# Kernel tuning notes

Hardware: AMD Instinct MI355X
Metric: run time of the kernel (lower is better)

## Reference

```python
import jax, jax.numpy as jnp
import numpy as np

NUM_HEADS = 12
HEAD_DIM = 32  # all_head_size(384) / num_heads(12)


def setup_inputs() -> dict:
    key = jax.random.key(0)
    ks = jax.random.split(key, 8)
    B, Sq, Sk, Din, AH = 1, 4096, 4096, 768, 384
    scale = 1.0 / np.sqrt(Din)
    return {
        "hidden_states": jax.random.normal(ks[0], (B, Sq, Din), jnp.float32),
        "encoder_hidden_states": jax.random.normal(ks[1], (B, Sk, Din), jnp.float32),
        "encoder_attention_mask": jnp.zeros((B, 1, 1, Sk), jnp.float32),
        "Wq": jax.random.normal(ks[2], (Din, AH), jnp.float32) * scale,
        "bq": jnp.zeros((AH,), jnp.float32),
        "Wk": jax.random.normal(ks[3], (Din, AH), jnp.float32) * scale,
        "bk": jnp.zeros((AH,), jnp.float32),
        "Wv": jax.random.normal(ks[4], (Din, AH), jnp.float32) * scale,
        "bv": jnp.zeros((AH,), jnp.float32),
    }


def _split_heads(x):
    # [B, S, H*D] -> [B, H, S, D]
    B, S, _ = x.shape
    return x.reshape(B, S, NUM_HEADS, HEAD_DIM).transpose(0, 2, 1, 3)


def reference(hidden_states, encoder_hidden_states, encoder_attention_mask,
              Wq, bq, Wk, bk, Wv, bv):
    q = _split_heads(hidden_states @ Wq + bq)            # [B,H,Sq,D]
    k = _split_heads(encoder_hidden_states @ Wk + bk)    # [B,H,Sk,D]
    v = _split_heads(encoder_hidden_states @ Wv + bv)    # [B,H,Sk,D]

    scores = jnp.einsum('bhqd,bhkd->bhqk', q, k) / np.sqrt(HEAD_DIM)
    scores = scores + encoder_attention_mask              # additive mask, broadcast
    probs = jax.nn.softmax(scores, axis=-1)               # dropout is identity (eval)

    ctx = jnp.einsum('bhqk,bhkd->bhqd', probs, v)         # [B,H,Sq,D]
    B, H, Sq, D = ctx.shape
    return ctx.transpose(0, 2, 1, 3).reshape(B, Sq, H * D)  # [B,Sq,all_head_size]
```

## Files before the change

kernel.cpp:

```cpp
#include <hip/hip_runtime.h>
#include <hip/hip_bf16.h>

#define SQ 4096
#define SKK 4096
#define DIN 768
#define AHS 384
#define NHEAD 12
#define HD 32

typedef __attribute__((ext_vector_type(8))) short bf16x8;
typedef __attribute__((ext_vector_type(4))) float f32x4;
typedef __attribute__((ext_vector_type(4))) unsigned int u32x4;

#define LOG2E 1.4426950408889634f
#define QSCALE 0.25503486168652855f

__device__ __forceinline__ unsigned short bf16_rn(float x){
  unsigned int u = __float_as_uint(x);
  unsigned int r = u + 0x7fffu + ((u>>16)&1u);
  return (unsigned short)(r>>16);
}
__device__ __forceinline__ float bf16_f(unsigned short h){
  return __uint_as_float(((unsigned int)h)<<16);
}
__device__ __forceinline__ float fexp2(float x){
#if __has_builtin(__builtin_amdgcn_exp2f)
  return __builtin_amdgcn_exp2f(x);
#else
  float r; asm("v_exp_f32 %0, %1" : "=v"(r) : "v"(x)); return r;
#endif
}

__global__ void prep_wt_kernel(const float* __restrict__ Wq, const float* __restrict__ Wk,
                               const float* __restrict__ Wv, const float* __restrict__ mask,
                               unsigned short* __restrict__ Wthi, unsigned short* __restrict__ Wtlo,
                               unsigned short* __restrict__ EMB){
  int idx = blockIdx.x*256 + threadIdx.x;
  if (idx < SKK) EMB[idx] = bf16_rn(__expf(mask[idx]));
  const int per = DIN*AHS;
  if (idx >= 3*per) return;
  int mat = idx/per, rem = idx - mat*per;
  int k = rem/AHS, n = rem - k*AHS;
  const float* W = (mat==0)?Wq:((mat==1)?Wk:Wv);
  float v = W[k*AHS+n];
  unsigned short hh = bf16_rn(v);
  unsigned short ll = bf16_rn(v - bf16_f(hh));
  Wthi[mat*per + n*DIN + k] = hh;
  Wtlo[mat*per + n*DIN + k] = ll;
}

__global__ __launch_bounds__(512,4) void proj2_kernel(
    const float* __restrict__ Xh, const float* __restrict__ Xe,
    const unsigned short* __restrict__ Wthi, const unsigned short* __restrict__ Wtlo,
    const float* __restrict__ bq, const float* __restrict__ bk, const float* __restrict__ bv,
    const unsigned short* __restrict__ EMB,
    unsigned short* __restrict__ Qhi, unsigned short* __restrict__ Qlo,
    unsigned short* __restrict__ Khi, unsigned short* __restrict__ Klo,
    unsigned short* __restrict__ Vt)
{
  const int z = blockIdx.z;
  const float* A = (z==0) ? Xh : Xe;
  const unsigned short* Bh = Wthi + (size_t)z*(DIN*AHS);
  const unsigned short* Bl = Wtlo + (size_t)z*(DIN*AHS);
  const float* bias = (z==0) ? bq : ((z==1) ? bk : bv);

  const int m0 = blockIdx.x*128;
  const int n0 = blockIdx.y*128;
  const int tid = threadIdx.x;
  const int w = tid>>6, lane = tid&63;
  const int lm = lane&15, g = lane>>4;
  const int wm = w>>1, wn = w&1;

  __shared__ __align__(16) unsigned short SH[32768];

  const int srow = tid>>2, scol = (tid&3)*8;
  const float* pA = A + (size_t)(m0 + srow)*DIN + scol;
  const size_t gb = (size_t)(n0 + srow)*DIN + scol;
  const int sidx = srow*32 + ((((tid&3) ^ ((srow>>1)&3)))<<3);

  f32x4 xa0, xa1; u32x4 rb, rlb;
  auto sload = [&](int kk){
    xa0 = *(const f32x4*)(pA + kk);
    xa1 = *(const f32x4*)(pA + kk + 4);
    rb  = *(const u32x4*)(Bh + gb + kk);
    if (z != 2) rlb = *(const u32x4*)(Bl + gb + kk);
  };
  auto swrite = [&](int b){
    float xx[8] = {xa0[0],xa0[1],xa0[2],xa0[3],xa1[0],xa1[1],xa1[2],xa1[3]};
    unsigned int hw[4];
    #pragma unroll
    for (int p=0;p<4;++p)
      asm("v_cvt_pk_bf16_f32 %0, %1, %2" : "=v"(hw[p]) : "v"(xx[2*p]), "v"(xx[2*p+1]));
    u32x4 ra = {hw[0],hw[1],hw[2],hw[3]};
    *(u32x4*)&SH[b*16384 + 0*4096 + sidx] = ra;
    *(u32x4*)&SH[b*16384 + 2*4096 + sidx] = rb;
    if (z != 2){
      unsigned int lw[4];
      #pragma unroll
      for (int p=0;p<4;++p){
        float h0 = __uint_as_float(hw[p]<<16);
        float h1 = __uint_as_float(hw[p] & 0xffff0000u);
        float l0 = xx[2*p] - h0, l1 = xx[2*p+1] - h1;
        asm("v_cvt_pk_bf16_f32 %0, %1, %2" : "=v"(lw[p]) : "v"(l0), "v"(l1));
      }
      u32x4 rla = {lw[0],lw[1],lw[2],lw[3]};
      *(u32x4*)&SH[b*16384 + 1*4096 + sidx] = rla;
      *(u32x4*)&SH[b*16384 + 3*4096 + sidx] = rlb;
    }
  };

  f32x4 acc[2][4];
  #pragma unroll
  for (int mi=0;mi<2;++mi)
    #pragma unroll
    for (int ni=0;ni<4;++ni) acc[mi][ni] = (f32x4){0.f,0.f,0.f,0.f};

  auto fidx = [&](int row)->int{ return row*32 + ((g ^ ((row>>1)&3))<<3); };

  sload(0); swrite(0); __syncthreads();
  int cur = 0;

  const int NKS = DIN/32;
  for (int t=0; t<NKS; ++t){
    if (t+1 < NKS) sload((t+1)*32);

    const unsigned short* AhL = &SH[cur*16384 + 0*4096];
    const unsigned short* AlL = &SH[cur*16384 + 1*4096];
    const unsigned short* BhL = &SH[cur*16384 + 2*4096];
    const unsigned short* BlL = &SH[cur*16384 + 3*4096];

    bf16x8 a0h = *(const bf16x8*)&AhL[fidx(wm*32 + lm)];
    bf16x8 a1h = *(const bf16x8*)&AhL[fidx(wm*32 + 16 + lm)];
    bf16x8 a0l, a1l;
    if (z != 2){
      a0l = *(const bf16x8*)&AlL[fidx(wm*32 + lm)];
      a1l = *(const bf16x8*)&AlL[fidx(wm*32 + 16 + lm)];
    }
    __builtin_amdgcn_s_setprio(1);
    #pragma unroll
    for (int ni=0; ni<4; ++ni){
      bf16x8 bh = *(const bf16x8*)&BhL[fidx(wn*64 + ni*16 + lm)];
      acc[0][ni] = __builtin_amdgcn_mfma_f32_16x16x32_bf16(a0h, bh, acc[0][ni], 0,0,0);
      acc[1][ni] = __builtin_amdgcn_mfma_f32_16x16x32_bf16(a1h, bh, acc[1][ni], 0,0,0);
      if (z != 2){
        bf16x8 bl = *(const bf16x8*)&BlL[fidx(wn*64 + ni*16 + lm)];
        acc[0][ni] = __builtin_amdgcn_mfma_f32_16x16x32_bf16(a0h, bl, acc[0][ni], 0,0,0);
        acc[1][ni] = __builtin_amdgcn_mfma_f32_16x16x32_bf16(a1h, bl, acc[1][ni], 0,0,0);
        acc[0][ni] = __builtin_amdgcn_mfma_f32_16x16x32_bf16(a0l, bh, acc[0][ni], 0,0,0);
        acc[1][ni] = __builtin_amdgcn_mfma_f32_16x16x32_bf16(a1l, bh, acc[1][ni], 0,0,0);
      }
    }
    __builtin_amdgcn_s_setprio(0);

    if (t+1 < NKS) swrite(cur^1);
    __syncthreads();
    cur ^= 1;
  }

  if (z != 2){
    #pragma unroll
    for (int ni=0; ni<4; ++ni){
      int col = n0 + wn*64 + ni*16 + lm;
      float bcol = bias[col];
      int hq = col>>5, d = col&31;
      #pragma unroll
      for (int mi=0; mi<2; ++mi){
        #pragma unroll
        for (int r=0; r<4; ++r){
          int row = m0 + wm*32 + mi*16 + g*4 + r;
          float v = acc[mi][ni][r] + bcol;
          if (z==0) v *= QSCALE;
          unsigned short hh = bf16_rn(v);
          unsigned short ll = bf16_rn(v - bf16_f(hh));
          size_t p = (z==0) ? ((size_t)hq*SQ + row)*HD + d
                            : ((size_t)hq*SKK + row)*HD + d;
          if (z==0){ Qhi[p]=hh; Qlo[p]=ll; } else { Khi[p]=hh; Klo[p]=ll; }
        }
      }
    }
  } else {
    #pragma unroll
    for (int ni=0; ni<4; ++ni){
      int lcol = wn*64 + ni*16 + lm;
      float bcol = bias[n0 + lcol];
      #pragma unroll
      for (int mi=0; mi<2; ++mi){
        #pragma unroll
        for (int r=0; r<4; ++r){
          int lrow = wm*32 + mi*16 + g*4 + r;
          float emf = bf16_f(EMB[m0 + lrow]);
          SH[lcol*128 + (lrow ^ ((lcol&7)<<3))] = bf16_rn((acc[mi][ni][r] + bcol) * emf);
        }
      }
    }
    __syncthreads();
    #pragma unroll
    for (int p=0; p<4; ++p){
      int c = tid>>2, rc = (tid&3)*8 + p*32;
      bf16x8 vv = *(const bf16x8*)&SH[c*128 + (rc ^ ((c&7)<<3))];
      *(bf16x8*)(Vt + (size_t)(n0 + c)*SKK + m0 + rc) = vv;
    }
  }
}

__global__ __launch_bounds__(256) void attn_kernel(
    const unsigned short* __restrict__ Qhi, const unsigned short* __restrict__ Qlo,
    const unsigned short* __restrict__ Khi, const unsigned short* __restrict__ Klo,
    const unsigned short* __restrict__ Vt, const unsigned short* __restrict__ EMB,
    float* __restrict__ opart, float* __restrict__ lpart,
    int nkt, int direct)
{
  const int qt = blockIdx.x, h = blockIdx.y, sp = blockIdx.z;
  const int tid = threadIdx.x;
  const int w = tid>>6, lane = tid&63;
  const int lm = lane&15, g = lane>>4;
  const int qrow = qt*64 + w*16 + lm;
  const int kbeg = sp*nkt*64;

  __shared__ unsigned short KhL[2][2048];
  __shared__ unsigned short KlL[2][2048];
  __shared__ unsigned short VL [2][2048];

  const int krow_s = tid>>2, kc = tid&3;
  const int ksw = ((krow_s>>1)&1) ^ (((krow_s>>3)&1)<<1);
  const int kds = krow_s*32 + ((kc ^ ksw)<<3);
  const int vrow_s = tid>>3;
  const int vds = vrow_s*64 + (((tid&7) ^ (vrow_s&7))<<3);

  const unsigned short* pKh = Khi + (size_t)h*SKK*HD + (size_t)(kbeg+krow_s)*HD + kc*8;
  const unsigned short* pKl = Klo + (size_t)h*SKK*HD + (size_t)(kbeg+krow_s)*HD + kc*8;
  const unsigned short* pV  = Vt + (size_t)(h*HD + vrow_s)*SKK + kbeg + (tid&7)*8;
  const unsigned short* pEM = EMB + kbeg + g*8;

  const int krs = ((lm>>2)<<3) + (lm&3);
  const int rsw = ((krs>>1)&1) ^ (((krs>>3)&1)<<1);
  const int kread0 = krs*32 + ((g ^ rsw)<<3);

  int vr[4];
  vr[0] = (lm*64      + g*8)      ^ ((lm&7)<<3);
  vr[1] = (lm*64      + 32 + g*8) ^ ((lm&7)<<3);
  vr[2] = ((lm+16)*64 + g*8)      ^ ((lm&7)<<3);
  vr[3] = ((lm+16)*64 + 32 + g*8) ^ ((lm&7)<<3);

  bf16x8 qh = *(const bf16x8*)(Qhi + ((size_t)h*SQ + qrow)*HD + g*8);
  bf16x8 ql = *(const bf16x8*)(Qlo + ((size_t)h*SQ + qrow)*HD + g*8);

  f32x4 o0 = {0.f,0.f,0.f,0.f}, o1 = {0.f,0.f,0.f,0.f};
  f32x4 lacc = {0.f,0.f,0.f,0.f};

  u32x4 sa = *(const u32x4*)pKh;
  u32x4 sb = *(const u32x4*)pKl;
  u32x4 sc = *(const u32x4*)pV;
  *(u32x4*)(&KhL[0][kds]) = sa;
  *(u32x4*)(&KlL[0][kds]) = sb;
  *(u32x4*)(&VL [0][vds]) = sc;
  __syncthreads();

  #pragma unroll 2
  for (int t=0; t<nkt; ++t){
    const int cur = t&1;

    if (t+1 < nkt){
      pKh += 64*HD; pKl += 64*HD; pV += 64;
      sa = *(const u32x4*)pKh;
      sb = *(const u32x4*)pKl;
      sc = *(const u32x4*)pV;
    }

    bf16x8 em0 = *(const bf16x8*)(pEM);
    bf16x8 em1 = *(const bf16x8*)(pEM + 32);
    pEM += 64;

    unsigned int wds[8];
    #pragma unroll
    for (int ks=0; ks<4; ++ks){
      const int kidx = kread0 + (ks&1)*128 + (ks>>1)*1024;
      bf16x8 kh = *(const bf16x8*)(&KhL[cur][kidx]);
      bf16x8 kl = *(const bf16x8*)(&KlL[cur][kidx]);
      f32x4 a = {0.f,0.f,0.f,0.f};
      __builtin_amdgcn_s_setprio(1);
      a = __builtin_amdgcn_mfma_f32_16x16x32_bf16(kh, qh, a, 0,0,0);
      a = __builtin_amdgcn_mfma_f32_16x16x32_bf16(kh, ql, a, 0,0,0);
      a = __builtin_amdgcn_mfma_f32_16x16x32_bf16(kl, qh, a, 0,0,0);
      __builtin_amdgcn_s_setprio(0);
      float p0 = fexp2(a[0]);
      float p1 = fexp2(a[1]);
      float p2 = fexp2(a[2]);
      float p3 = fexp2(a[3]);
      asm("v_cvt_pk_bf16_f32 %0, %1, %2" : "=v"(wds[ks*2])   : "v"(p0), "v"(p1));
      asm("v_cvt_pk_bf16_f32 %0, %1, %2" : "=v"(wds[ks*2+1]) : "v"(p2), "v"(p3));
    }
    u32x4 w0v = {wds[0], wds[1], wds[2], wds[3]};
    u32x4 w1v = {wds[4], wds[5], wds[6], wds[7]};
    bf16x8 pa0 = __builtin_bit_cast(bf16x8, w0v);
    bf16x8 pa1 = __builtin_bit_cast(bf16x8, w1v);

    bf16x8 v00 = *(const bf16x8*)(&VL[cur][vr[0]]);
    bf16x8 v01 = *(const bf16x8*)(&VL[cur][vr[1]]);
    bf16x8 v10 = *(const bf16x8*)(&VL[cur][vr[2]]);
    bf16x8 v11 = *(const bf16x8*)(&VL[cur][vr[3]]);
    __builtin_amdgcn_s_setprio(1);
    o0   = __builtin_amdgcn_mfma_f32_16x16x32_bf16(pa0, v00, o0,   0,0,0);
    o1   = __builtin_amdgcn_mfma_f32_16x16x32_bf16(pa0, v10, o1,   0,0,0);
    lacc = __builtin_amdgcn_mfma_f32_16x16x32_bf16(pa0, em0, lacc, 0,0,0);
    o0   = __builtin_amdgcn_mfma_f32_16x16x32_bf16(pa1, v01, o0,   0,0,0);
    o1   = __builtin_amdgcn_mfma_f32_16x16x32_bf16(pa1, v11, o1,   0,0,0);
    lacc = __builtin_amdgcn_mfma_f32_16x16x32_bf16(pa1, em1, lacc, 0,0,0);
    __builtin_amdgcn_s_setprio(0);

    if (t+1 < nkt){
      *(u32x4*)(&KhL[cur^1][kds]) = sa;
      *(u32x4*)(&KlL[cur^1][kds]) = sb;
      *(u32x4*)(&VL [cur^1][vds]) = sc;
    }
    __syncthreads();
  }

  if (direct){
    #pragma unroll
    for (int r=0;r<4;++r){
      float inv = 1.0f / lacc[r];
      int row = qt*64 + w*16 + g*4 + r;
      opart[(size_t)row*AHS + h*HD + lm]      = o0[r]*inv;
      opart[(size_t)row*AHS + h*HD + 16 + lm] = o1[r]*inv;
    }
  } else {
    #pragma unroll
    for (int r=0;r<4;++r){
      int row = qt*64 + w*16 + g*4 + r;
      opart[((size_t)sp*SQ + row)*AHS + h*HD + lm]      = o0[r];
      opart[((size_t)sp*SQ + row)*AHS + h*HD + 16 + lm] = o1[r];
    }
    if (lm == 0){
      #pragma unroll
      for (int r=0;r<4;++r){
        int row = qt*64 + w*16 + g*4 + r;
        lpart[((size_t)sp*NHEAD + h)*SQ + row] = lacc[r];
      }
    }
  }
}

__global__ void merge_kernel(const float* __restrict__ opart,
                             const float* __restrict__ lpart,
                             float* __restrict__ out, int S){
  int idx = blockIdx.x*256 + threadIdx.x;
  if (idx >= SQ*AHS) return;
  int row = idx/AHS, c = idx - row*AHS;
  int h = c >> 5;
  float num = 0.f, den = 0.f;
  for (int s=0; s<S; ++s){
    num += opart[((size_t)s*SQ + row)*AHS + c];
    den += lpart[((size_t)s*NHEAD + h)*SQ + row];
  }
  out[idx] = num/den;
}

extern "C" void kernel_launch(void* const* d_in, const int* in_sizes, int n_in,
                              void* d_out, int out_size, void* d_ws, size_t ws_size,
                              hipStream_t stream) {
  const float* Xh   = (const float*)d_in[0];
  const float* Xe   = (const float*)d_in[1];
  const float* mask = (const float*)d_in[2];
  const float* Wq   = (const float*)d_in[3];
  const float* bq   = (const float*)d_in[4];
  const float* Wk   = (const float*)d_in[5];
  const float* bk   = (const float*)d_in[6];
  const float* Wv   = (const float*)d_in[7];
  const float* bv   = (const float*)d_in[8];
  float* out = (float*)d_out;

  char* ws = (char*)d_ws;
  auto al256 = [](size_t b)->size_t{ return (b + 255) & ~(size_t)255; };
  size_t off = 0;
  auto alloc = [&](size_t bytes)->void*{ void* p = ws + off; off += al256(bytes); return p; };

  unsigned short* Wthi = (unsigned short*)alloc((size_t)3*DIN*AHS*2);
  unsigned short* Wtlo = (unsigned short*)alloc((size_t)3*DIN*AHS*2);
  unsigned short* EMB  = (unsigned short*)alloc((size_t)SKK*2);
  unsigned short* Qhi  = (unsigned short*)alloc((size_t)NHEAD*SQ*HD*2);
  unsigned short* Qlo  = (unsigned short*)alloc((size_t)NHEAD*SQ*HD*2);
  unsigned short* Khi  = (unsigned short*)alloc((size_t)NHEAD*SKK*HD*2);
  unsigned short* Klo  = (unsigned short*)alloc((size_t)NHEAD*SKK*HD*2);
  unsigned short* Vt   = (unsigned short*)alloc((size_t)AHS*SKK*2);
  const size_t base_end = off;

  const size_t OB = al256((size_t)SQ*AHS*4);
  const size_t MB = al256((size_t)NHEAD*SQ*4);

  auto fits = [&](int S)->bool{
    return base_end + (size_t)S*OB + (size_t)S*MB + 8192 <= ws_size;
  };

  int S = 1, direct = 0;
  if      (fits(4)) S = 4;
  else if (fits(2)) S = 2;
  else if (fits(1)) S = 1;
  else { S = 1; direct = 1; }

  char* ureg = ws + base_end;
  float *opart, *lpart;
  if (!direct){
    opart = (float*)(ureg);
    lpart = (float*)(ureg + (size_t)S*OB);
  } else {
    opart = out; lpart = (float*)ws;
  }

  {
    int tot = 3*DIN*AHS;
    prep_wt_kernel<<<(tot+255)/256, 256, 0, stream>>>(Wq, Wk, Wv, mask, Wthi, Wtlo, EMB);
  }
  {
    dim3 grid(SQ/128, AHS/128, 3);
    proj2_kernel<<<grid, 512, 0, stream>>>(Xh, Xe, Wthi, Wtlo,
                                           bq, bk, bv, EMB, Qhi, Qlo, Khi, Klo, Vt);
  }
  {
    dim3 grid(SQ/64, NHEAD, S);
    int nkt = (SKK/64)/S;
    attn_kernel<<<grid, 256, 0, stream>>>(Qhi, Qlo, Khi, Klo, Vt, EMB,
                                          opart, lpart, nkt, direct);
  }
  if (!direct){
    int n = SQ*AHS;
    merge_kernel<<<(n+255)/256, 256, 0, stream>>>(opart, lpart, out, S);
  }
}
```

Measured before the change: 117.5 us.

## Use direct global-to-LDS loads, XCD-aware block remap, and tiled weight transpose

The attention kernel now stages K/V tiles with global_load_lds instead of going through registers, and pre-swizzles the global addresses so the LDS layout matches the old XOR layout. The attention and projection grids are flattened and remapped so consecutive logical blocks land on the same XCD, which improves L2 reuse of K/V and weights. Weight preparation is split out from the mask-exp kernel and uses an LDS-tiled transpose so its stores are coalesced. The projection launch bound also drops from 4 to 2 blocks per CU. Risks include the hard-coded remap constants (8 XCDs, chunk sizes) and the LDS layout correctness of the direct-load path.

Result: faster. 113.2 us (-3.7%).

```diff
diff --git a/kernel.cpp b/kernel.cpp
--- a/kernel.cpp
+++ b/kernel.cpp
@@ -15,6 +15,10 @@
 #define LOG2E 1.4426950408889634f
 #define QSCALE 0.25503486168652855f
 
+#define GLD16(gp, lp) __builtin_amdgcn_global_load_lds( \
+    (const __attribute__((address_space(1))) void*)(gp), \
+    (__attribute__((address_space(3))) void*)(lp), 16, 0, 0)
+
 __device__ __forceinline__ unsigned short bf16_rn(float x){
   unsigned int u = __float_as_uint(x);
   unsigned int r = u + 0x7fffu + ((u>>16)&1u);
@@ -31,25 +35,53 @@
 #endif
 }
 
-__global__ void prep_wt_kernel(const float* __restrict__ Wq, const float* __restrict__ Wk,
-                               const float* __restrict__ Wv, const float* __restrict__ mask,
-                               unsigned short* __restrict__ Wthi, unsigned short* __restrict__ Wtlo,
-                               unsigned short* __restrict__ EMB){
+__global__ void em_kernel(const float* __restrict__ mask, unsigned short* __restrict__ EMB){
   int idx = blockIdx.x*256 + threadIdx.x;
   if (idx < SKK) EMB[idx] = bf16_rn(__expf(mask[idx]));
-  const int per = DIN*AHS;
-  if (idx >= 3*per) return;
-  int mat = idx/per, rem = idx - mat*per;
-  int k = rem/AHS, n = rem - k*AHS;
-  const float* W = (mat==0)?Wq:((mat==1)?Wk:Wv);
-  float v = W[k*AHS+n];
-  unsigned short hh = bf16_rn(v);
-  unsigned short ll = bf16_rn(v - bf16_f(hh));
-  Wthi[mat*per + n*DIN + k] = hh;
-  Wtlo[mat*per + n*DIN + k] = ll;
-}
-
-__global__ __launch_bounds__(512,4) void proj2_kernel(
+}
+
+__global__ __launch_bounds__(256) void prep2_kernel(
+    const float* __restrict__ Wq, const float* __restrict__ Wk, const float* __restrict__ Wv,
+    unsigned short* __restrict__ Wthi, unsigned short* __restrict__ Wtlo)
+{
+  const int z = blockIdx.z;
+  const float* W = (z==0)?Wq:((z==1)?Wk:Wv);
+  const int k0 = blockIdx.x*64, n0 = blockIdx.y*64;
+  const int tid = threadIdx.x;
+
+  __shared__ float T[64][65];
+
+  const int kr = tid>>2, nc = (tid&3)*16;
+  const float* src = W + (size_t)(k0+kr)*AHS + n0 + nc;
+  #pragma unroll
+  for (int p=0; p<4; ++p){
+    f32x4 v = *(const f32x4*)(src + p*4);
+    T[kr][nc + p*4 + 0] = v[0];
+    T[kr][nc + p*4 + 1] = v[1];
+    T[kr][nc + p*4 + 2] = v[2];
+    T[kr][nc + p*4 + 3] = v[3];
+  }
+  __syncthreads();
+
+  const int nr = tid>>2, ks = (tid&3)*16;
+  unsigned short* dh = Wthi + (size_t)(z*AHS + n0 + nr)*DIN + k0 + ks;
+  unsigned short* dl = Wtlo + (size_t)(z*AHS + n0 + nr)*DIN + k0 + ks;
+  #pragma unroll
+  for (int half=0; half<2; ++half){
+    bf16x8 hv, lv;
+    #pragma unroll
+    for (int j=0; j<8; ++j){
+      float v = T[ks + half*8 + j][nr];
+      unsigned short hh = bf16_rn(v);
+      hv[j] = (short)hh;
+      lv[j] = (short)bf16_rn(v - bf16_f(hh));
+    }
+    *(bf16x8*)(dh + half*8) = hv;
+    *(bf16x8*)(dl + half*8) = lv;
+  }
+}
+
+__global__ __launch_bounds__(512,2) void proj5_kernel(
     const float* __restrict__ Xh, const float* __restrict__ Xe,
     const unsigned short* __restrict__ Wthi, const unsigned short* __restrict__ Wtlo,
     const float* __restrict__ bq, const float* __restrict__ bk, const float* __restrict__ bv,
@@ -58,14 +90,19 @@
     unsigned short* __restrict__ Khi, unsigned short* __restrict__ Klo,
     unsigned short* __restrict__ Vt)
 {
-  const int z = blockIdx.z;
+  const int bid = blockIdx.x;
+  const int logical = (bid & 7)*36 + (bid >> 3);
+  const int mb = logical & 31;
+  const int rest = logical >> 5;
+  const int nb = rest % 3, z = rest / 3;
+
   const float* A = (z==0) ? Xh : Xe;
   const unsigned short* Bh = Wthi + (size_t)z*(DIN*AHS);
   const unsigned short* Bl = Wtlo + (size_t)z*(DIN*AHS);
   const float* bias = (z==0) ? bq : ((z==1) ? bk : bv);
 
-  const int m0 = blockIdx.x*128;
-  const int n0 = blockIdx.y*128;
+  const int m0 = mb*128;
+  const int n0 = nb*128;
   const int tid = threadIdx.x;
   const int w = tid>>6, lane = tid&63;
   const int lm = lane&15, g = lane>>4;
@@ -73,10 +110,10 @@
 
   __shared__ __align__(16) unsigned short SH[32768];
 
-  const int srow = tid>>2, scol = (tid&3)*8;
-  const float* pA = A + (size_t)(m0 + srow)*DIN + scol;
-  const size_t gb = (size_t)(n0 + srow)*DIN + scol;
-  const int sidx = srow*32 + ((((tid&3) ^ ((srow>>1)&3)))<<3);
+  const int srow = tid>>2, scn = tid&3;
+  const int sidx = srow*32 + ((scn ^ ((srow>>1)&3))<<3);
+  const float* pA = A + (size_t)(m0 + srow)*DIN + scn*8;
+  const size_t gb = (size_t)(n0 + srow)*DIN + scn*8;
 
   f32x4 xa0, xa1; u32x4 rb, rlb;
   auto sload = [&](int kk){
@@ -208,9 +245,14 @@
     const unsigned short* __restrict__ Khi, const unsigned short* __restrict__ Klo,
     const unsigned short* __restrict__ Vt, const unsigned short* __restrict__ EMB,
     float* __restrict__ opart, float* __restrict__ lpart,
-    int nkt, int direct)
+    int nkt, int direct, int chunk)
 {
-  const int qt = blockIdx.x, h = blockIdx.y, sp = blockIdx.z;
+  const int bid = blockIdx.x;
+  const int logical = (bid & 7)*chunk + (bid >> 3);
+  const int qt = logical & 63;
+  const int rest = logical >> 6;
+  const int h = rest % NHEAD, sp = rest / NHEAD;
+
   const int tid = threadIdx.x;
   const int w = tid>>6, lane = tid&63;
   const int lm = lane&15, g = lane>>4;
@@ -221,15 +263,15 @@
   __shared__ unsigned short KlL[2][2048];
   __shared__ unsigned short VL [2][2048];
 
-  const int krow_s = tid>>2, kc = tid&3;
-  const int ksw = ((krow_s>>1)&1) ^ (((krow_s>>3)&1)<<1);
-  const int kds = krow_s*32 + ((kc ^ ksw)<<3);
-  const int vrow_s = tid>>3;
-  const int vds = vrow_s*64 + (((tid&7) ^ (vrow_s&7))<<3);
-
-  const unsigned short* pKh = Khi + (size_t)h*SKK*HD + (size_t)(kbeg+krow_s)*HD + kc*8;
-  const unsigned short* pKl = Klo + (size_t)h*SKK*HD + (size_t)(kbeg+krow_s)*HD + kc*8;
-  const unsigned short* pV  = Vt + (size_t)(h*HD + vrow_s)*SKK + kbeg + (tid&7)*8;
+  const int krow_l = 16*w + (lane>>2);
+  const int ksw_l = ((krow_l>>1)&1) ^ (((krow_l>>3)&1)<<1);
+  const unsigned short* gKh = Khi + (size_t)h*SKK*HD
+                            + (size_t)(kbeg + krow_l)*HD + (((lane&3)^ksw_l)<<3);
+  const unsigned short* gKl = Klo + (size_t)h*SKK*HD
+                            + (size_t)(kbeg + krow_l)*HD + (((lane&3)^ksw_l)<<3);
+  const int vrow_l = 8*w + (lane>>3);
+  const unsigned short* gV = Vt + (size_t)(h*HD + vrow_l)*SKK + kbeg
+                           + (((lane&7)^(lane>>3))<<3);
   const unsigned short* pEM = EMB + kbeg + g*8;
 
   const int krs = ((lm>>2)<<3) + (lm&3);
@@ -248,12 +290,9 @@
   f32x4 o0 = {0.f,0.f,0.f,0.f}, o1 = {0.f,0.f,0.f,0.f};
   f32x4 lacc = {0.f,0.f,0.f,0.f};
 
-  u32x4 sa = *(const u32x4*)pKh;
-  u32x4 sb = *(const u32x4*)pKl;
-  u32x4 sc = *(const u32x4*)pV;
-  *(u32x4*)(&KhL[0][kds]) = sa;
-  *(u32x4*)(&KlL[0][kds]) = sb;
-  *(u32x4*)(&VL [0][vds]) = sc;
+  GLD16(gKh, &KhL[0][w*512]);
+  GLD16(gKl, &KlL[0][w*512]);
+  GLD16(gV,  &VL [0][w*512]);
   __syncthreads();
 
   #pragma unroll 2
@@ -261,10 +300,10 @@
     const int cur = t&1;
 
     if (t+1 < nkt){
-      pKh += 64*HD; pKl += 64*HD; pV += 64;
-      sa = *(const u32x4*)pKh;
-      sb = *(const u32x4*)pKl;
-      sc = *(const u32x4*)pV;
+      gKh += 64*HD; gKl += 64*HD; gV += 64;
+      GLD16(gKh, &KhL[cur^1][w*512]);
+      GLD16(gKl, &KlL[cur^1][w*512]);
+      GLD16(gV,  &VL [cur^1][w*512]);
     }
 
     bf16x8 em0 = *(const bf16x8*)(pEM);
@@ -308,11 +347,6 @@
     lacc = __builtin_amdgcn_mfma_f32_16x16x32_bf16(pa1, em1, lacc, 0,0,0);
     __builtin_amdgcn_s_setprio(0);
 
-    if (t+1 < nkt){
-      *(u32x4*)(&KhL[cur^1][kds]) = sa;
-      *(u32x4*)(&KlL[cur^1][kds]) = sb;
-      *(u32x4*)(&VL [cur^1][vds]) = sc;
-    }
     __syncthreads();
   }
 
@@ -408,19 +442,19 @@
   }
 
   {
-    int tot = 3*DIN*AHS;
-    prep_wt_kernel<<<(tot+255)/256, 256, 0, stream>>>(Wq, Wk, Wv, mask, Wthi, Wtlo, EMB);
+    em_kernel<<<(SKK+255)/256, 256, 0, stream>>>(mask, EMB);
+    dim3 grid(DIN/64, AHS/64, 3);
+    prep2_kernel<<<grid, 256, 0, stream>>>(Wq, Wk, Wv, Wthi, Wtlo);
   }
   {
-    dim3 grid(SQ/128, AHS/128, 3);
-    proj2_kernel<<<grid, 512, 0, stream>>>(Xh, Xe, Wthi, Wtlo,
-                                           bq, bk, bv, EMB, Qhi, Qlo, Khi, Klo, Vt);
+    proj5_kernel<<<288, 512, 0, stream>>>(Xh, Xe, Wthi, Wtlo,
+                                          bq, bk, bv, EMB, Qhi, Qlo, Khi, Klo, Vt);
   }
   {
-    dim3 grid(SQ/64, NHEAD, S);
+    int nblk = 64*NHEAD*S;
     int nkt = (SKK/64)/S;
-    attn_kernel<<<grid, 256, 0, stream>>>(Qhi, Qlo, Khi, Klo, Vt, EMB,
-                                          opart, lpart, nkt, direct);
+    attn_kernel<<<nblk, 256, 0, stream>>>(Qhi, Qlo, Khi, Klo, Vt, EMB,
+                                          opart, lpart, nkt, direct, nblk/8);
   }
   if (!direct){
     int n = SQ*AHS;
```
